# Optimization experiments

Hardware: AMD Instinct MI355X
Metric: run time of the kernel (lower is better)

Reference implementation:

```python
import jax, jax.numpy as jnp
import numpy as np

B, C, W, F, NC = 512, 12, 4, 512, 4  # batch, leads, windows(=4, hardcoded by conv0), features, classes


def setup_inputs() -> dict:
    key = jax.random.key(0)
    ks = jax.random.split(key, 16)
    g = lambda i, shape, s=1.0: jax.random.normal(ks[i], shape, jnp.float32) * s
    return {
        "x": g(0, (B, C, W, F)),
        # GRU (PyTorch layout: W_ih [3F,F], W_hh [3F,F], gate order r,z,n)
        "gru_wih": g(1, (3 * F, F), 0.03),
        "gru_whh": g(2, (3 * F, F), 0.03),
        "gru_bih": jnp.zeros((3 * F,), jnp.float32),
        "gru_bhh": jnp.zeros((3 * F,), jnp.float32),
        # GraphLearning 1x1 convs (squeezed kernels); positive biases keep adj nondegenerate
        "conv0_w": g(3, (W,), 0.5), "conv0_b": jnp.float32(0.1),
        "conv1_w": g(4, (F,), 0.05), "conv1_b": jnp.float32(0.1),
        "conv2_w": g(5, (C * C, C), 0.3),
        "conv2_b": 0.1 + 0.05 * jnp.abs(g(6, (C * C,))),
        # GCN stack
        "gcn_w": g(7, (2, F, F), 0.04), "gcn_b": jnp.zeros((2, F), jnp.float32),
        # classifier head (jax [in,out] layout); BN in eval mode
        "fc1_w": g(8, (C * F, 512), 0.02), "fc1_b": jnp.zeros((512,), jnp.float32),
        "bn1_g": jnp.ones((512,), jnp.float32), "bn1_b": jnp.zeros((512,), jnp.float32),
        "bn1_m": 0.1 * g(9, (512,)), "bn1_v": 1.0 + 0.1 * jnp.abs(g(10, (512,))),
        "fc2_w": g(11, (512, 512), 0.04), "fc2_b": jnp.zeros((512,), jnp.float32),
        "bn2_g": jnp.ones((512,), jnp.float32), "bn2_b": jnp.zeros((512,), jnp.float32),
        "bn2_m": 0.1 * g(12, (512,)), "bn2_v": 1.0 + 0.1 * jnp.abs(g(13, (512,))),
        "fc3_w": g(14, (512, NC), 0.04), "fc3_b": jnp.zeros((NC,), jnp.float32),
    }


def reference(x, gru_wih, gru_whh, gru_bih, gru_bhh,
              conv0_w, conv0_b, conv1_w, conv1_b, conv2_w, conv2_b,
              gcn_w, gcn_b,
              fc1_w, fc1_b, bn1_g, bn1_b, bn1_m, bn1_v,
              fc2_w, fc2_b, bn2_g, bn2_b, bn2_m, bn2_v,
              fc3_w, fc3_b):
    b, c, w, f = x.shape
    # --- GRU over leads dim; each window slice starts from h0=0, so merge (batch, w) ---
    xs = x.transpose(0, 2, 1, 3).reshape(b * w, c, f)            # [N, C, F]
    xW = jnp.einsum('ntf,gf->ntg', xs, gru_wih) + gru_bih        # precompute input gates [N,C,3F]

    def step(h, xw_t):
        hg = h @ gru_whh.T + gru_bhh
        xr, xz, xn = jnp.split(xw_t, 3, axis=-1)
        hr, hz, hn = jnp.split(hg, 3, axis=-1)
        r = jax.nn.sigmoid(xr + hr)
        z = jax.nn.sigmoid(xz + hz)
        n = jnp.tanh(xn + r * hn)
        h = (1.0 - z) * n + z * h
        return h, h

    _, hs = jax.lax.scan(step, jnp.zeros((b * w, f), x.dtype), xW.transpose(1, 0, 2))
    gru_out = hs.transpose(1, 0, 2).reshape(b, w, c, f).transpose(0, 2, 1, 3)  # [B,C,W,F]

    # --- GraphLearning: 1x1 convs -> 12x12 adjacency -> normalized Laplacian -> Chebyshev K=4 ---
    g0 = gru_out.transpose(0, 2, 1, 3)                               # [B,W,C,F]
    y = jax.nn.relu(jnp.einsum('bwcf,w->bcf', g0, conv0_w) + conv0_b)  # [B,C,F]
    y = jax.nn.relu(jnp.einsum('bcf,f->bc', y, conv1_w) + conv1_b)     # [B,C]
    y = jax.nn.relu(jnp.einsum('bc,kc->bk', y, conv2_w) + conv2_b)     # [B,C*C]
    a = jnp.mean(y.reshape(b, c, c), axis=0)
    adj = jax.nn.relu(a)
    degree = jnp.sum(adj, axis=1)
    adj_s = 0.5 * (adj + adj.T)
    d_hat = 1.0 / (jnp.sqrt(degree) + 1e-7)
    lap = d_hat[:, None] * (jnp.diag(degree) - adj_s) * d_hat[None, :]
    L0 = jnp.zeros_like(lap)
    L1 = lap
    L2 = 2.0 * lap @ L1 - L0
    L3 = 2.0 * lap @ L2 - L1
    cheb = jnp.stack([L0, L1, L2, L3], axis=0)                       # [4,C,C]

    # --- GCN stack with residuals (dropout is identity in eval) ---
    h = gru_out.transpose(0, 2, 1, 3)[:, :, None]                    # [B,W,1,C,F]
    tmp = h
    res = h
    for i in range(gcn_w.shape[0]):
        support = jnp.einsum('bwocf,fg->bwocg', h, gcn_w[i])
        out = jnp.einsum('wij,bwojf->bwoif', cheb, support) + gcn_b[i]
        h = jax.nn.relu(out) + res
        res = h
    h = tmp + h
    h = h[:, :, 0].sum(1).reshape(b, c * f)                          # [B, C*F]

    # --- classifier head (eval-mode BN, dropout identity) ---
    def bn(v, gmm, bt, m, var):
        return (v - m) / jnp.sqrt(var + 1e-5) * gmm + bt

    h = bn(jax.nn.leaky_relu(h @ fc1_w + fc1_b, 0.01), bn1_g, bn1_b, bn1_m, bn1_v)
    h = bn(jax.nn.leaky_relu(h @ fc2_w + fc2_b, 0.01), bn2_g, bn2_b, bn2_m, bn2_v)
    return h @ fc3_w + fc3_b
```

## Files before the change

kernel.cpp:

```cpp
#include <hip/hip_runtime.h>
#include <cmath>

constexpr int Bb  = 512;
constexpr int Cc  = 12;
constexpr int Ww  = 4;
constexpr int Ff  = 512;
constexpr int Mx  = Bb * Ww * Cc;

typedef __attribute__((ext_vector_type(8))) short bf16x8;
typedef __attribute__((ext_vector_type(4))) float f32x4;

__device__ __forceinline__ float sigm(float v) { return 1.f / (1.f + expf(-v)); }
__device__ __forceinline__ float b2f(ushort u) { union { float f; unsigned i; } v; v.i = ((unsigned)u) << 16; return v.f; }
__device__ __forceinline__ ushort f2b(float f) {
    union { float f; unsigned i; } v; v.f = f;
    unsigned r = v.i + 0x7FFFu + ((v.i >> 16) & 1u);
    return (ushort)(r >> 16);
}
__device__ __forceinline__ void async16(const ushort* g, ushort* l) {
    __builtin_amdgcn_global_load_lds(
        (const __attribute__((address_space(1))) unsigned int*)g,
        (__attribute__((address_space(3))) unsigned int*)l, 16, 0, 0);
}

__global__ __launch_bounds__(256) void mfma_gemm(
    const ushort* __restrict__ A, const ushort* __restrict__ Bt,
    float* __restrict__ Cf, ushort* __restrict__ Cb,
    const float* __restrict__ colBias,
    int N, int K, int kLen, int MN, int gridY)
{
    __shared__ ushort As[128 * 64], Bs[128 * 64];
    const int tid = threadIdx.x;
    const int ln = tid & 63, wv = tid >> 6;
    const int l = blockIdx.x;
    const int by = l % gridY, bx = l / gridY, bz = blockIdx.y;
    const int srow = ln >> 3;
    const int kslot = (ln & 7) ^ srow;
    const int rowA0 = by * 128 + wv * 32;
    const int rowB0 = bx * 128 + wv * 32;
    const ushort* ga = A  + (long)(rowA0 + srow) * K + bz * kLen + kslot * 8;
    const ushort* gb = Bt + (long)(rowB0 + srow) * K + bz * kLen + kslot * 8;
    ushort* la = As + wv * 32 * 64;
    ushort* lb = Bs + wv * 32 * 64;
    const int rbase = (wv >> 1) * 64, cbase = (wv & 1) * 64;
    const int mrow = ln & 15, quad = ln >> 4;

    f32x4 acc[4][4] = {};

    for (int kc = 0; kc < kLen; kc += 64) {
        #pragma unroll
        for (int i = 0; i < 4; ++i) {
            async16(ga + (long)(i * 8) * K, la + i * 8 * 64);
            async16(gb + (long)(i * 8) * K, lb + i * 8 * 64);
        }
        ga += 64; gb += 64;
        __syncthreads();
        #pragma unroll
        for (int s = 0; s < 2; ++s) {
            const int sw = (((s << 2) + quad) ^ (ln & 7)) << 3;
            bf16x8 af[4], bf[4];
            #pragma unroll
            for (int i = 0; i < 4; ++i)
                af[i] = *(const bf16x8*)(As + (rbase + i * 16 + mrow) * 64 + sw);
            #pragma unroll
            for (int j = 0; j < 4; ++j)
                bf[j] = *(const bf16x8*)(Bs + (cbase + j * 16 + mrow) * 64 + sw);
            #pragma unroll
            for (int i = 0; i < 4; ++i)
                #pragma unroll
                for (int j = 0; j < 4; ++j)
                    acc[i][j] = __builtin_amdgcn_mfma_f32_16x16x32_bf16(bf[j], af[i], acc[i][j], 0, 0, 0);
        }
        __syncthreads();
    }

    const int gr0 = by * 128 + rbase + mrow;
    const int gc0 = bx * 128 + cbase + quad * 4;
    if (Cb) {
        #pragma unroll
        for (int i = 0; i < 4; ++i) {
            const long rowoff = (long)(gr0 + i * 16) * N;
            #pragma unroll
            for (int j = 0; j < 4; ++j) {
                float c0 = 0.f, c1 = 0.f, c2 = 0.f, c3 = 0.f;
                if (colBias) {
                    const float4 cb4 = *(const float4*)(colBias + gc0 + j * 16);
                    c0 = cb4.x; c1 = cb4.y; c2 = cb4.z; c3 = cb4.w;
                }
                union { ushort u[4]; uint2 v; } pk;
                pk.u[0] = f2b(acc[i][j][0] + c0);
                pk.u[1] = f2b(acc[i][j][1] + c1);
                pk.u[2] = f2b(acc[i][j][2] + c2);
                pk.u[3] = f2b(acc[i][j][3] + c3);
                *(uint2*)&Cb[rowoff + gc0 + j * 16] = pk.v;
            }
        }
    } else {
        float* Co = Cf + (long)bz * MN;
        #pragma unroll
        for (int i = 0; i < 4; ++i) {
            const long rowoff = (long)(gr0 + i * 16) * N;
            #pragma unroll
            for (int j = 0; j < 4; ++j)
                *(f32x4*)&Co[rowoff + gc0 + j * 16] = acc[i][j];
        }
    }
}

__global__ __launch_bounds__(512, 1) void gru_persist(
    const ushort* __restrict__ xW, const ushort* __restrict__ whhB,
    const float* __restrict__ bih, const float* __restrict__ bhh,
    ushort* __restrict__ h0, ushort* __restrict__ h1,
    ushort* __restrict__ G, unsigned* __restrict__ bar)
{
    __shared__ ushort Bw[8 * 96 * 64];
    __shared__ ushort Ah[2][128 * 64];
    const int tid = threadIdx.x, ln = tid & 63, wv = tid >> 6;
    const int mb = blockIdx.x & 15, fb = blockIdx.x >> 4;
    const int srow = ln >> 3, kslot = (ln & 7) ^ srow;
    const int mrow = ln & 15, quad = ln >> 4;

    #pragma unroll
    for (int i = 0; i < 12; ++i) {
        const int rg = i * 8 + wv;
        const int kc6 = rg / 12, rgi = rg - kc6 * 12;
        const int r0 = rgi * 8, r = r0 + srow;
        const int g = r >> 5, fc = r & 31;
        async16(whhB + (long)(g * 512 + fb * 32 + fc) * 512 + kc6 * 64 + kslot * 8,
                Bw + (kc6 * 96 + r0) * 64);
    }

    float br[2][4], bz[2][4], bni[2][4], bnh[2][4];
    #pragma unroll
    for (int ft = 0; ft < 2; ++ft) {
        const int f0 = fb * 32 + ft * 16 + quad * 4;
        const float4 bir = *(const float4*)(bih + f0);
        const float4 biz = *(const float4*)(bih + 512 + f0);
        const float4 bin = *(const float4*)(bih + 1024 + f0);
        const float4 bhr = *(const float4*)(bhh + f0);
        const float4 bhz = *(const float4*)(bhh + 512 + f0);
        const float4 bhn = *(const float4*)(bhh + 1024 + f0);
        br[ft][0] = bir.x + bhr.x; br[ft][1] = bir.y + bhr.y; br[ft][2] = bir.z + bhr.z; br[ft][3] = bir.w + bhr.w;
        bz[ft][0] = biz.x + bhz.x; bz[ft][1] = biz.y + bhz.y; bz[ft][2] = biz.z + bhz.z; bz[ft][3] = biz.w + bhz.w;
        bni[ft][0] = bin.x; bni[ft][1] = bin.y; bni[ft][2] = bin.z; bni[ft][3] = bin.w;
        bnh[ft][0] = bhn.x; bnh[ft][1] = bhn.y; bnh[ft][2] = bhn.z; bnh[ft][3] = bhn.w;
    }
    __syncthreads();

    const int n = mb * 128 + wv * 16 + mrow;
    const long nrow = (long)n * 512;
    unsigned* cptr = bar + mb * 16;

    const int c0r = tid >> 3,          c0k = tid & 7;
    const int c1r = (tid + 512) >> 3,  c1k = tid & 7;
    const int s0  = c0k ^ (c0r & 7),   s1 = c1k ^ (c1r & 7);

    uint2 hprev[2]; hprev[0].x = 0u; hprev[0].y = 0u; hprev[1] = hprev[0];

    for (int t = 0; t < 12; ++t) {
        const ushort* hin = (t & 1) ? h1 : h0;
        ushort* hout = (t & 1) ? h0 : h1;
        f32x4 acc[6] = {};

        const long xrow = ((long)n * 12 + t) * 1536;
        uint2 xrv[2], xzv[2], xnv[2];
        #pragma unroll
        for (int ft = 0; ft < 2; ++ft) {
            const int f0 = fb * 32 + ft * 16 + quad * 4;
            xrv[ft] = *(const uint2*)(xW + xrow + f0);
            xzv[ft] = *(const uint2*)(xW + xrow + 512 + f0);
            xnv[ft] = *(const uint2*)(xW + xrow + 1024 + f0);
        }

        if (t > 0) {
            const ushort* hb = hin + (long)(mb * 128) * 512;
            unsigned long long hr0[8][2], hr1[8][2];
            {
                const ushort* b0 = hb + (long)c0r * 512 + c0k * 8;
                const ushort* b1 = hb + (long)c1r * 512 + c1k * 8;
                #pragma unroll
                for (int k6 = 0; k6 < 8; ++k6) {
                    hr0[k6][0] = __hip_atomic_load((const unsigned long long*)(b0 + k6 * 64),
                                                   __ATOMIC_RELAXED, __HIP_MEMORY_SCOPE_AGENT);
                    hr0[k6][1] = __hip_atomic_load((const unsigned long long*)(b0 + k6 * 64 + 4),
                                                   __ATOMIC_RELAXED, __HIP_MEMORY_SCOPE_AGENT);
                    hr1[k6][0] = __hip_atomic_load((const unsigned long long*)(b1 + k6 * 64),
                                                   __ATOMIC_RELAXED, __HIP_MEMORY_SCOPE_AGENT);
                    hr1[k6][1] = __hip_atomic_load((const unsigned long long*)(b1 + k6 * 64 + 4),
                                                   __ATOMIC_RELAXED, __HIP_MEMORY_SCOPE_AGENT);
                }
            }
            {
                ulonglong2 v0; v0.x = hr0[0][0]; v0.y = hr0[0][1];
                ulonglong2 v1; v1.x = hr1[0][0]; v1.y = hr1[0][1];
                *(ulonglong2*)(Ah[0] + c0r * 64 + s0 * 8) = v0;
                *(ulonglong2*)(Ah[0] + c1r * 64 + s1 * 8) = v1;
            }
            __syncthreads();
            #pragma unroll
            for (int k6 = 0; k6 < 8; ++k6) {
                if (k6 < 7) {
                    ulonglong2 v0; v0.x = hr0[k6 + 1][0]; v0.y = hr0[k6 + 1][1];
                    ulonglong2 v1; v1.x = hr1[k6 + 1][0]; v1.y = hr1[k6 + 1][1];
                    *(ulonglong2*)(Ah[(k6 + 1) & 1] + c0r * 64 + s0 * 8) = v0;
                    *(ulonglong2*)(Ah[(k6 + 1) & 1] + c1r * 64 + s1 * 8) = v1;
                }
                const ushort* Bk = Bw + k6 * (96 * 64);
                const ushort* Ak = Ah[k6 & 1];
                #pragma unroll
                for (int s = 0; s < 2; ++s) {
                    const int sw = (((s << 2) + quad) ^ (ln & 7)) << 3;
                    const bf16x8 ah = *(const bf16x8*)(Ak + (wv * 16 + mrow) * 64 + sw);
                    #pragma unroll
                    for (int jt = 0; jt < 6; ++jt) {
                        const bf16x8 bh = *(const bf16x8*)(Bk + (jt * 16 + mrow) * 64 + sw);
                        acc[jt] = __builtin_amdgcn_mfma_f32_16x16x32_bf16(bh, ah, acc[jt], 0, 0, 0);
                    }
                }
                __syncthreads();
            }
        }

        #pragma unroll
        for (int ft = 0; ft < 2; ++ft) {
            const int f0 = fb * 32 + ft * 16 + quad * 4;
            const ushort* xr = (const ushort*)&xrv[ft];
            const ushort* xz = (const ushort*)&xzv[ft];
            const ushort* xn = (const ushort*)&xnv[ft];
            const ushort* hp = (const ushort*)&hprev[ft];
            union { ushort u[4]; uint2 v; unsigned long long q; } o;
            #pragma unroll
            for (int r = 0; r < 4; ++r) {
                const float rr = sigm(acc[ft][r] + b2f(xr[r]) + br[ft][r]);
                const float zz = sigm(acc[2 + ft][r] + b2f(xz[r]) + bz[ft][r]);
                const float nv = tanhf(b2f(xn[r]) + bni[ft][r] + rr * (acc[4 + ft][r] + bnh[ft][r]));
                o.u[r] = f2b((1.f - zz) * nv + zz * b2f(hp[r]));
            }
            hprev[ft] = o.v;
            __hip_atomic_store((unsigned long long*)&hout[nrow + f0], o.q,
                               __ATOMIC_RELAXED, __HIP_MEMORY_SCOPE_AGENT);
            *(uint2*)&G[((long)n * 12 + t) * 512 + f0] = o.v;
        }

        if (t < 11) {
            asm volatile("s_waitcnt vmcnt(0)" ::: "memory");
            __syncthreads();
            if (tid == 0) {
                __hip_atomic_fetch_add(cptr, 1u, __ATOMIC_RELAXED, __HIP_MEMORY_SCOPE_AGENT);
                const unsigned tgt = (unsigned)(t + 1) * 16u;
                while (__hip_atomic_load(cptr, __ATOMIC_RELAXED, __HIP_MEMORY_SCOPE_AGENT) < tgt)
                    __builtin_amdgcn_s_sleep(1);
            }
            __syncthreads();
        }
    }
}

__global__ __launch_bounds__(256) void cvt_x(const float* __restrict__ x, ushort* __restrict__ xb)
{
    const int idx = blockIdx.x * 256 + threadIdx.x;
    const int m = idx >> 6, f8 = (idx & 63) << 3;
    const int n = m / 12, c = m - n * 12;
    const int b = n >> 2, w = n & 3;
    const float* src = x + (((b * 12 + c) * 4 + w) << 9) + f8;
    const float4 a = *(const float4*)src, q = *(const float4*)(src + 4);
    uint4 o;
    o.x = (unsigned)f2b(a.x) | ((unsigned)f2b(a.y) << 16);
    o.y = (unsigned)f2b(a.z) | ((unsigned)f2b(a.w) << 16);
    o.z = (unsigned)f2b(q.x) | ((unsigned)f2b(q.y) << 16);
    o.w = (unsigned)f2b(q.z) | ((unsigned)f2b(q.w) << 16);
    *(uint4*)(xb + (m << 9) + f8) = o;
}

__global__ __launch_bounds__(256) void cvt_w2(
    const float* __restrict__ wih, const float* __restrict__ whh,
    ushort* __restrict__ wihB, ushort* __restrict__ whhB)
{
    int bx = blockIdx.x;
    const float* s; ushort* d;
    if (bx < 384) { s = wih; d = wihB; } else { s = whh; d = whhB; bx -= 384; }
    const int e = (bx * 256 + threadIdx.x) << 3;
    const float4 a = *(const float4*)(s + e), q = *(const float4*)(s + e + 4);
    uint4 o;
    o.x = (unsigned)f2b(a.x) | ((unsigned)f2b(a.y) << 16);
    o.y = (unsigned)f2b(a.z) | ((unsigned)f2b(a.w) << 16);
    o.z = (unsigned)f2b(q.x) | ((unsigned)f2b(q.y) << 16);
    o.w = (unsigned)f2b(q.z) | ((unsigned)f2b(q.w) << 16);
    *(uint4*)(d + e) = o;
}

__global__ __launch_bounds__(256) void tcvt_all(
    const float* __restrict__ gcnw, const float* __restrict__ f1w, const float* __restrict__ f2w,
    ushort* __restrict__ gw0, ushort* __restrict__ gw1,
    ushort* __restrict__ f1t, ushort* __restrict__ f2t)
{
    int by = blockIdx.y;
    const float* src; ushort* dst; int R, C;
    if (by < 16)       { src = gcnw;          dst = gw0; R = 512;  C = 512; }
    else if (by < 32)  { src = gcnw + 262144; dst = gw1; R = 512;  C = 512; by -= 16; }
    else if (by < 224) { src = f1w;           dst = f1t; R = 6144; C = 512; by -= 32; }
    else               { src = f2w;           dst = f2t; R = 512;  C = 512; by -= 224; }
    __shared__ float tl[32][33];
    const int c0 = blockIdx.x * 32, r0 = by * 32;
    const int cx = threadIdx.x & 31, ry = threadIdx.x >> 5;
    #pragma unroll
    for (int k = 0; k < 4; ++k) tl[ry + k * 8][cx] = src[(long)(r0 + ry + k * 8) * C + c0 + cx];
    __syncthreads();
    #pragma unroll
    for (int k = 0; k < 4; ++k) dst[(long)(c0 + ry + k * 8) * R + r0 + cx] = f2b(tl[cx][ry + k * 8]);
}

__global__ __launch_bounds__(256) void conv01(
    const ushort* __restrict__ G, const float* __restrict__ w0, const float* __restrict__ b0,
    const float* __restrict__ w1, const float* __restrict__ b1, float* __restrict__ y2)
{
    const int row = (blockIdx.x * 256 + threadIdx.x) >> 6;
    const int lane = threadIdx.x & 63;
    const int b = row / 12, c = row - 12 * b;
    const float w00 = w0[0], w01 = w0[1], w02 = w0[2], w03 = w0[3], bb = b0[0];
    const ushort* gp = G + ((long)(b * 4) * 12 + c) * 512;
    float s = 0.f;
    for (int f = lane; f < 512; f += 64) {
        const float v = bb + b2f(gp[f]) * w00 + b2f(gp[6144 + f]) * w01
                      + b2f(gp[12288 + f]) * w02 + b2f(gp[18432 + f]) * w03;
        s += fmaxf(v, 0.f) * w1[f];
    }
    #pragma unroll
    for (int off = 32; off; off >>= 1) s += __shfl_down(s, off);
    if (lane == 0) y2[row] = fmaxf(s + b1[0], 0.f);
}

__global__ __launch_bounds__(256) void conv2_cheb(
    const float* __restrict__ y2, const float* __restrict__ w2,
    const float* __restrict__ b2, float* __restrict__ cheb)
{
    __shared__ float ys[6144];
    __shared__ float adj[144], deg[12], dhat[12], lap[144], T2[144];
    const int tid = threadIdx.x;
    for (int i = tid; i < 6144; i += 256) ys[i] = y2[i];
    __syncthreads();
    if (tid < 144) {
        float wk[12];
        #pragma unroll
        for (int c = 0; c < 12; ++c) wk[c] = w2[tid * 12 + c];
        const float bias = b2[tid];
        float s = 0.f;
        for (int b = 0; b < 512; ++b) {
            float v = bias;
            #pragma unroll
            for (int c = 0; c < 12; ++c) v += ys[b * 12 + c] * wk[c];
            s += fmaxf(v, 0.f);
        }
        adj[tid] = fmaxf(s * (1.f / 512.f), 0.f);
    }
    __syncthreads();
    if (tid < 12) {
        float s = 0.f;
        for (int j = 0; j < 12; ++j) s += adj[tid * 12 + j];
        deg[tid] = s; dhat[tid] = 1.f / (sqrtf(s) + 1e-7f);
    }
    __syncthreads();
    if (tid < 144) {
        const int i = tid / 12, j = tid % 12;
        const float as = 0.5f * (adj[i * 12 + j] + adj[j * 12 + i]);
        lap[tid] = dhat[i] * ((i == j ? deg[i] : 0.f) - as) * dhat[j];
    }
    __syncthreads();
    if (tid < 144) {
        const int i = tid / 12, j = tid % 12;
        float s = 0.f;
        for (int kk = 0; kk < 12; ++kk) s += lap[i * 12 + kk] * lap[kk * 12 + j];
        T2[tid] = 2.f * s;
    }
    __syncthreads();
    if (tid < 144) {
        const int i = tid / 12, j = tid % 12;
        float s = 0.f;
        for (int kk = 0; kk < 12; ++kk) s += lap[i * 12 + kk] * T2[kk * 12 + j];
        cheb[tid] = 0.f;
        cheb[144 + tid] = lap[tid];
        cheb[288 + tid] = T2[tid];
        cheb[432 + tid] = 2.f * s - lap[tid];
    }
}

__global__ __launch_bounds__(256) void gcn_epi1(
    const ushort* __restrict__ S, const float* __restrict__ cheb,
    const float* __restrict__ gcnb, const ushort* __restrict__ G,
    ushort* __restrict__ H1)
{
    __shared__ float ch[576];
    const int tid = threadIdx.x;
    for (int i = tid; i < 576; i += 256) ch[i] = cheb[i];
    __syncthreads();
    const int idx = blockIdx.x * 256 + tid;
    const int f = idx & 511, bc = idx >> 9;
    const int b = bc / 12, c = bc - 12 * b;
    const float bias = gcnb[f];
    #pragma unroll
    for (int w = 0; w < 4; ++w) {
        float o = bias;
        const ushort* Sr = S + ((b * 4 + w) * 12) * 512 + f;
        const float* cw = ch + w * 144 + c * 12;
        #pragma unroll
        for (int j = 0; j < 12; ++j) o += cw[j] * b2f(Sr[j * 512]);
        const int gi = ((b * 4 + w) * 12 + c) * 512 + f;
        H1[gi] = f2b(fmaxf(o, 0.f) + b2f(G[gi]));
    }
}

__global__ __launch_bounds__(256) void gcn_epi2(
    const ushort* __restrict__ S, const float* __restrict__ cheb,
    const float* __restrict__ gcnb, const ushort* __restrict__ G,
    const ushort* __restrict__ H1, ushort* __restrict__ pooled)
{
    __shared__ float ch[576];
    const int tid = threadIdx.x;
    for (int i = tid; i < 576; i += 256) ch[i] = cheb[i];
    __syncthreads();
    const int idx = blockIdx.x * 256 + tid;
    const int f = idx & 511, bc = idx >> 9;
    const int b = bc / 12, c = bc - 12 * b;
    const float bias = gcnb[f];
    float acc = 0.f;
    #pragma unroll
    for (int w = 0; w < 4; ++w) {
        float o = bias;
        const ushort* Sr = S + ((b * 4 + w) * 12) * 512 + f;
        const float* cw = ch + w * 144 + c * 12;
        #pragma unroll
        for (int j = 0; j < 12; ++j) o += cw[j] * b2f(Sr[j * 512]);
        const int gi = ((b * 4 + w) * 12 + c) * 512 + f;
        acc += fmaxf(o, 0.f) + b2f(H1[gi]) + b2f(G[gi]);
    }
    pooled[idx] = f2b(acc);
}

__global__ __launch_bounds__(256) void fc_epi(
    const float* __restrict__ part, int nsplit, const float* __restrict__ bias,
    const float* __restrict__ g, const float* __restrict__ be,
    const float* __restrict__ mu, const float* __restrict__ var,
    ushort* __restrict__ outb, float* __restrict__ outf)
{
    const int idx = blockIdx.x * 256 + threadIdx.x;
    const int c = idx & 511;
    float s = bias[c];
    for (int k = 0; k < nsplit; ++k) s += part[k * 262144 + idx];
    s = s >= 0.f ? s : 0.01f * s;
    s = (s - mu[c]) * rsqrtf(var[c] + 1e-5f) * g[c] + be[c];
    if (outb) outb[idx] = f2b(s); else outf[idx] = s;
}

__global__ __launch_bounds__(256) void fc3_kernel(
    const float* __restrict__ z2, const float* __restrict__ w3,
    const float* __restrict__ b3, float* __restrict__ out)
{
    const int idx = blockIdx.x * 256 + threadIdx.x;
    const int m = idx >> 2, nc = idx & 3;
    float s = b3[nc];
    const float* zr = z2 + m * 512;
    for (int k = 0; k < 512; ++k) s += zr[k] * w3[k * 4 + nc];
    out[idx] = s;
}

extern "C" void kernel_launch(void* const* d_in, const int* in_sizes, int n_in,
                              void* d_out, int out_size, void* d_ws, size_t ws_size,
                              hipStream_t stream)
{
    (void)in_sizes; (void)n_in; (void)out_size; (void)ws_size;
    const float* x    = (const float*)d_in[0];
    const float* wih  = (const float*)d_in[1];
    const float* whh  = (const float*)d_in[2];
    const float* bih  = (const float*)d_in[3];
    const float* bhh  = (const float*)d_in[4];
    const float* c0w  = (const float*)d_in[5];
    const float* c0b  = (const float*)d_in[6];
    const float* c1w  = (const float*)d_in[7];
    const float* c1b  = (const float*)d_in[8];
    const float* c2w  = (const float*)d_in[9];
    const float* c2b  = (const float*)d_in[10];
    const float* gcnw = (const float*)d_in[11];
    const float* gcnb = (const float*)d_in[12];
    const float* f1w  = (const float*)d_in[13];
    const float* f1b  = (const float*)d_in[14];
    const float* bn1g = (const float*)d_in[15];
    const float* bn1b = (const float*)d_in[16];
    const float* bn1m = (const float*)d_in[17];
    const float* bn1v = (const float*)d_in[18];
    const float* f2w  = (const float*)d_in[19];
    const float* f2b_ = (const float*)d_in[20];
    const float* bn2g = (const float*)d_in[21];
    const float* bn2b = (const float*)d_in[22];
    const float* bn2m = (const float*)d_in[23];
    const float* bn2v = (const float*)d_in[24];
    const float* f3w  = (const float*)d_in[25];
    const float* f3b  = (const float*)d_in[26];

    char* W = (char*)d_ws;
    ushort* xW     = (ushort*)(W + 0);
    ushort* S      = (ushort*)(W + 0);
    ushort* H1     = (ushort*)(W + 25165824);
    ushort* pooled = (ushort*)(W + 50331648);
    float*  z1p    = (float*)(W + 58720256);
    float*  z2p    = z1p;
    ushort* xb     = (ushort*)(W + 75497472);
    ushort* G      = (ushort*)(W + 75497472);
    ushort* h0     = (ushort*)(W + 100663296);
    ushort* h1     = (ushort*)(W + 102760448);
    ushort* whhB   = (ushort*)(W + 104857600);
    ushort* wihB   = (ushort*)(W + 106430464);
    ushort* gw0    = (ushort*)(W + 108003328);
    ushort* gw1    = (ushort*)(W + 108527616);
    ushort* f1t    = (ushort*)(W + 109051904);
    ushort* f2t    = (ushort*)(W + 115343360);
    ushort* z1b    = (ushort*)(W + 115867648);
    float*  z2     = (float*)(W + 116391936);
    float*  y2     = (float*)(W + 117440512);
    float*  chebb  = (float*)(W + 117465088);
    unsigned* bar  = (unsigned*)(W + 117467392);

    hipMemsetAsync(bar, 0, 1024, stream);
    cvt_x<<<(Mx * 64) / 256, 256, 0, stream>>>(x, xb);
    cvt_w2<<<768, 256, 0, stream>>>(wih, whh, wihB, whhB);
    tcvt_all<<<dim3(16, 240), 256, 0, stream>>>(gcnw, f1w, f2w, gw0, gw1, f1t, f2t);

    mfma_gemm<<<dim3(2304, 1), 256, 0, stream>>>(
        xb, wihB, nullptr, xW, nullptr, 3 * Ff, Ff, Ff, 0, 192);
    gru_persist<<<256, 512, 0, stream>>>(xW, whhB, bih, bhh, h0, h1, G, bar);

    conv01<<<(Bb * Cc * 64) / 256, 256, 0, stream>>>(G, c0w, c0b, c1w, c1b, y2);
    conv2_cheb<<<1, 256, 0, stream>>>(y2, c2w, c2b, chebb);

    mfma_gemm<<<dim3(768, 1), 256, 0, stream>>>(
        G, gw0, nullptr, S, nullptr, Ff, Ff, Ff, 0, 192);
    gcn_epi1<<<(Bb * Cc * Ff) / 256, 256, 0, stream>>>(S, chebb, gcnb, G, H1);

    mfma_gemm<<<dim3(768, 1), 256, 0, stream>>>(
        H1, gw1, nullptr, S, nullptr, Ff, Ff, Ff, 0, 192);
    gcn_epi2<<<(Bb * Cc * Ff) / 256, 256, 0, stream>>>(S, chebb, gcnb + Ff, G, H1, pooled);

    mfma_gemm<<<dim3(16, 16), 256, 0, stream>>>(
        pooled, f1t, z1p, nullptr, nullptr, 512, Cc * Ff, 384, 262144, 4);
    fc_epi<<<1024, 256, 0, stream>>>(z1p, 16, f1b, bn1g, bn1b, bn1m, bn1v, z1b, nullptr);
    mfma_gemm<<<dim3(16, 4), 256, 0, stream>>>(
        z1b, f2t, z2p, nullptr, nullptr, 512, 512, 128, 262144, 4);
    fc_epi<<<1024, 256, 0, stream>>>(z2p, 4, f2b_, bn2g, bn2b, bn2m, bn2v, nullptr, z2);
    fc3_kernel<<<(Bb * 4) / 256, 256, 0, stream>>>(z2, f3w, f3b, (float*)d_out);
}
```

Baseline: 512.9 us.

## Store GRU hidden state in a fragment-blocked layout and overlap G writes with barrier

```diff
diff --git a/kernel.cpp b/kernel.cpp
--- a/kernel.cpp
+++ b/kernel.cpp
@@ -148,12 +148,22 @@
     __syncthreads();
 
     const int n = mb * 128 + wv * 16 + mrow;
-    const long nrow = (long)n * 512;
     unsigned* cptr = bar + mb * 16;
 
-    const int c0r = tid >> 3,          c0k = tid & 7;
-    const int c1r = (tid + 512) >> 3,  c1k = tid & 7;
-    const int s0  = c0k ^ (c0r & 7),   s1 = c1k ^ (c1r & 7);
+    const int st0 = (mb * 256 + (wv * 16 + fb) * 2 + 0) * 256 + (mrow * 4 + quad) * 4;
+    const int st1 = st0 + 256;
+
+    const int u1 = tid + 512;
+    const int awv0 = tid >> 7, afbi0 = (tid >> 6) & 1, aft0 = (tid >> 5) & 1, aj0 = tid & 31;
+    const int awv1 = u1 >> 7,  afbi1 = (u1 >> 6) & 1,  aft1 = (u1 >> 5) & 1,  aj1 = u1 & 31;
+    const int ar0 = awv0 * 16 + (aj0 >> 1);
+    const int ac0 = ((afbi0 * 4 + aft0 * 2 + (aj0 & 1)) ^ (ar0 & 7));
+    const int ad0 = ar0 * 64 + ac0 * 8;
+    const int ar1 = awv1 * 16 + (aj1 >> 1);
+    const int ac1 = ((afbi1 * 4 + aft1 * 2 + (aj1 & 1)) ^ (ar1 & 7));
+    const int ad1 = ar1 * 64 + ac1 * 8;
+    const int ag0 = mb * 65536 + ((awv0 * 16 + afbi0) * 2 + aft0) * 256 + aj0 * 8;
+    const int ag1 = mb * 65536 + ((awv1 * 16 + afbi1) * 2 + aft1) * 256 + aj1 * 8;
 
     uint2 hprev[2]; hprev[0].x = 0u; hprev[0].y = 0u; hprev[1] = hprev[0];
 
@@ -173,40 +183,37 @@
         }
 
         if (t > 0) {
-            const ushort* hb = hin + (long)(mb * 128) * 512;
-            unsigned long long hr0[8][2], hr1[8][2];
-            {
-                const ushort* b0 = hb + (long)c0r * 512 + c0k * 8;
-                const ushort* b1 = hb + (long)c1r * 512 + c1k * 8;
-                #pragma unroll
-                for (int k6 = 0; k6 < 8; ++k6) {
-                    hr0[k6][0] = __hip_atomic_load((const unsigned long long*)(b0 + k6 * 64),
-                                                   __ATOMIC_RELAXED, __HIP_MEMORY_SCOPE_AGENT);
-                    hr0[k6][1] = __hip_atomic_load((const unsigned long long*)(b0 + k6 * 64 + 4),
-                                                   __ATOMIC_RELAXED, __HIP_MEMORY_SCOPE_AGENT);
-                    hr1[k6][0] = __hip_atomic_load((const unsigned long long*)(b1 + k6 * 64),
-                                                   __ATOMIC_RELAXED, __HIP_MEMORY_SCOPE_AGENT);
-                    hr1[k6][1] = __hip_atomic_load((const unsigned long long*)(b1 + k6 * 64 + 4),
-                                                   __ATOMIC_RELAXED, __HIP_MEMORY_SCOPE_AGENT);
-                }
+            unsigned long long ha[8][2][2];
+            #pragma unroll
+            for (int kc = 0; kc < 8; ++kc) {
+                const ushort* p0 = hin + ag0 + kc * 1024;
+                const ushort* p1 = hin + ag1 + kc * 1024;
+                ha[kc][0][0] = __hip_atomic_load((const unsigned long long*)p0,
+                                                 __ATOMIC_RELAXED, __HIP_MEMORY_SCOPE_AGENT);
+                ha[kc][0][1] = __hip_atomic_load((const unsigned long long*)(p0 + 4),
+                                                 __ATOMIC_RELAXED, __HIP_MEMORY_SCOPE_AGENT);
+                ha[kc][1][0] = __hip_atomic_load((const unsigned long long*)p1,
+                                                 __ATOMIC_RELAXED, __HIP_MEMORY_SCOPE_AGENT);
+                ha[kc][1][1] = __hip_atomic_load((const unsigned long long*)(p1 + 4),
+                                                 __ATOMIC_RELAXED, __HIP_MEMORY_SCOPE_AGENT);
             }
             {
-                ulonglong2 v0; v0.x = hr0[0][0]; v0.y = hr0[0][1];
-                ulonglong2 v1; v1.x = hr1[0][0]; v1.y = hr1[0][1];
-                *(ulonglong2*)(Ah[0] + c0r * 64 + s0 * 8) = v0;
-                *(ulonglong2*)(Ah[0] + c1r * 64 + s1 * 8) = v1;
+                ulonglong2 v0; v0.x = ha[0][0][0]; v0.y = ha[0][0][1];
+                ulonglong2 v1; v1.x = ha[0][1][0]; v1.y = ha[0][1][1];
+                *(ulonglong2*)(Ah[0] + ad0) = v0;
+                *(ulonglong2*)(Ah[0] + ad1) = v1;
             }
             __syncthreads();
             #pragma unroll
-            for (int k6 = 0; k6 < 8; ++k6) {
-                if (k6 < 7) {
-                    ulonglong2 v0; v0.x = hr0[k6 + 1][0]; v0.y = hr0[k6 + 1][1];
-                    ulonglong2 v1; v1.x = hr1[k6 + 1][0]; v1.y = hr1[k6 + 1][1];
-                    *(ulonglong2*)(Ah[(k6 + 1) & 1] + c0r * 64 + s0 * 8) = v0;
-                    *(ulonglong2*)(Ah[(k6 + 1) & 1] + c1r * 64 + s1 * 8) = v1;
+            for (int kc = 0; kc < 8; ++kc) {
+                if (kc < 7) {
+                    ulonglong2 v0; v0.x = ha[kc + 1][0][0]; v0.y = ha[kc + 1][0][1];
+                    ulonglong2 v1; v1.x = ha[kc + 1][1][0]; v1.y = ha[kc + 1][1][1];
+                    *(ulonglong2*)(Ah[(kc + 1) & 1] + ad0) = v0;
+                    *(ulonglong2*)(Ah[(kc + 1) & 1] + ad1) = v1;
                 }
-                const ushort* Bk = Bw + k6 * (96 * 64);
-                const ushort* Ak = Ah[k6 & 1];
+                const ushort* Bk = Bw + kc * (96 * 64);
+                const ushort* Ak = Ah[kc & 1];
                 #pragma unroll
                 for (int s = 0; s < 2; ++s) {
                     const int sw = (((s << 2) + quad) ^ (ln & 7)) << 3;
@@ -223,12 +230,11 @@
 
         #pragma unroll
         for (int ft = 0; ft < 2; ++ft) {
-            const int f0 = fb * 32 + ft * 16 + quad * 4;
             const ushort* xr = (const ushort*)&xrv[ft];
             const ushort* xz = (const ushort*)&xzv[ft];
             const ushort* xn = (const ushort*)&xnv[ft];
             const ushort* hp = (const ushort*)&hprev[ft];
-            union { ushort u[4]; uint2 v; unsigned long long q; } o;
+            union { ushort u[4]; uint2 v; } o;
             #pragma unroll
             for (int r = 0; r < 4; ++r) {
                 const float rr = sigm(acc[ft][r] + b2f(xr[r]) + br[ft][r]);
@@ -237,16 +243,29 @@
                 o.u[r] = f2b((1.f - zz) * nv + zz * b2f(hp[r]));
             }
             hprev[ft] = o.v;
-            __hip_atomic_store((unsigned long long*)&hout[nrow + f0], o.q,
+        }
+
+        if (t < 11) {
+            union { uint2 v; unsigned long long q; } q0, q1;
+            q0.v = hprev[0]; q1.v = hprev[1];
+            __hip_atomic_store((unsigned long long*)&hout[st0], q0.q,
                                __ATOMIC_RELAXED, __HIP_MEMORY_SCOPE_AGENT);
-            *(uint2*)&G[((long)n * 12 + t) * 512 + f0] = o.v;
-        }
-
-        if (t < 11) {
+            __hip_atomic_store((unsigned long long*)&hout[st1], q1.q,
+                               __ATOMIC_RELAXED, __HIP_MEMORY_SCOPE_AGENT);
             asm volatile("s_waitcnt vmcnt(0)" ::: "memory");
             __syncthreads();
+            if (tid == 0)
+                __hip_atomic_fetch_add(cptr, 1u, __ATOMIC_RELAXED, __HIP_MEMORY_SCOPE_AGENT);
+        }
+
+        {
+            const int f0 = fb * 32 + quad * 4;
+            *(uint2*)&G[((long)n * 12 + t) * 512 + f0] = hprev[0];
+            *(uint2*)&G[((long)n * 12 + t) * 512 + f0 + 16] = hprev[1];
+        }
+
+        if (t < 11) {
             if (tid == 0) {
-                __hip_atomic_fetch_add(cptr, 1u, __ATOMIC_RELAXED, __HIP_MEMORY_SCOPE_AGENT);
                 const unsigned tgt = (unsigned)(t + 1) * 16u;
                 while (__hip_atomic_load(cptr, __ATOMIC_RELAXED, __HIP_MEMORY_SCOPE_AGENT) < tgt)
                     __builtin_amdgcn_s_sleep(1);
```

Result: no change. 518.7 us (+1.1%).
